# Optimization experiments

Hardware: AMD Instinct MI355X
Metric: run time of the kernel (lower is better)

Reference implementation:

```python
import jax, jax.numpy as jnp
import numpy as np

BLOCK_SIZE = 50  # from module globals


def setup_inputs() -> dict:
    key = jax.random.key(0)
    ks = jax.random.split(key, 5)
    B, T, C, H = 8, 1024, 512, 64
    return {
        "x": jax.random.normal(ks[0], (B, T, C), dtype=jnp.float32),
        "Wq": jax.random.normal(ks[1], (C, H), dtype=jnp.float32) * (C ** -0.5),
        "Wk": jax.random.normal(ks[2], (C, H), dtype=jnp.float32) * (C ** -0.5),
        "Wv": jax.random.normal(ks[3], (C, H), dtype=jnp.float32) * (C ** -0.5),
        "rel_pos_emb": jax.random.normal(ks[4], (2 * BLOCK_SIZE - 1, H), dtype=jnp.float32),
    }


def reference(x, Wq, Wk, Wv, rel_pos_emb):
    # x: [B, T, C]; dropout is identity in eval mode.
    B, T, C = x.shape
    q = x @ Wq  # [B, T, H]
    k = x @ Wk
    v = x @ Wv
    H = q.shape[-1]

    # relative position indices, clamped to window, shifted to [0, 2*block-2]
    t = jnp.arange(T)
    rel = jnp.clip(t[None, :] - t[:, None], -(BLOCK_SIZE - 1), BLOCK_SIZE - 1) + (BLOCK_SIZE - 1)
    E = rel_pos_emb[rel]  # [T, T, H]

    scale = H ** -0.5
    # content scores (scaled) + relative-position bias (unscaled, per source)
    wei = jnp.einsum("btd,bsd->bts", q, k) * scale + jnp.einsum("btd,tsd->bts", q, E)

    causal = t[None, :] <= t[:, None]  # [T, T] lower-triangular True
    wei = jnp.where(causal[None, :, :], wei, -jnp.inf)
    wei = jax.nn.softmax(wei, axis=-1)
    return jnp.einsum("bts,bsd->btd", wei, v)
```

## Files before the change

kernel.cpp:

```cpp
#include <hip/hip_runtime.h>
#include <hip/hip_bf16.h>

typedef __bf16 bf16x8 __attribute__((ext_vector_type(8)));
typedef float  f32x4  __attribute__((ext_vector_type(4)));

#define MFMA16(a, b, c) __builtin_amdgcn_mfma_f32_16x16x32_bf16(a, b, c, 0, 0, 0)

static __device__ __forceinline__ unsigned short bf16_bits(__bf16 v) {
    union { __bf16 b; unsigned short u; } x; x.b = v; return x.u;
}
static __device__ __forceinline__ f32x4 zero4() {
    f32x4 z = {0.f, 0.f, 0.f, 0.f}; return z;
}

__global__ void g_build_kernel(const float* __restrict__ Wq,
                               const float* __restrict__ rpe,
                               float* __restrict__ G) {
    int gid = blockIdx.x * 256 + threadIdx.x;
    int c = gid >> 6, j = gid & 63;
    const f32x4* wp = (const f32x4*)(Wq + c * 64);
    const f32x4* rp = (const f32x4*)(rpe + j * 64);
    float acc = 0.f;
#pragma unroll
    for (int i = 0; i < 16; i++) {
        f32x4 a = wp[i], b = rp[i];
        acc += a.x * b.x + a.y * b.y + a.z * b.z + a.w * b.w;
    }
    G[c * 64 + j] = acc;
}

__global__ void wt_build_kernel(const float* __restrict__ Wq,
                                const float* __restrict__ Wk,
                                const float* __restrict__ Wv,
                                const float* __restrict__ G,
                                __bf16* __restrict__ WT_hi,
                                __bf16* __restrict__ WT_lo) {
    int n = blockIdx.x;
    const float* src; int nc;
    if (n < 64)       { src = Wq; nc = n; }
    else if (n < 128) { src = Wk; nc = n - 64; }
    else if (n < 192) { src = Wv; nc = n - 128; }
    else              { src = G;  nc = n - 192; }
    int k = threadIdx.x * 2;
    float v0 = src[k * 64 + nc];
    float v1 = src[(k + 1) * 64 + nc];
    __bf16 h0 = (__bf16)v0, h1 = (__bf16)v1;
    WT_hi[n * 512 + k]     = h0;
    WT_hi[n * 512 + k + 1] = h1;
    WT_lo[n * 512 + k]     = (__bf16)(v0 - (float)h0);
    WT_lo[n * 512 + k + 1] = (__bf16)(v1 - (float)h1);
}

__global__ __launch_bounds__(256) void proj_kernel(
        const float* __restrict__ x,
        const __bf16* __restrict__ WT_hi, const __bf16* __restrict__ WT_lo,
        __bf16* __restrict__ qb, __bf16* __restrict__ kb,
        __bf16* __restrict__ vb, float* __restrict__ qE) {
    int tid = threadIdx.x;
    int lane = tid & 63, w = tid >> 6;
    int rt = w >> 1, ns = w & 1;
    int l15 = lane & 15, kg = lane >> 4;
    int rowA = blockIdx.x * 32 + rt * 16 + l15;
    const float* xrow = x + (size_t)rowA * 512;

    f32x4 acc[8];
#pragma unroll
    for (int i = 0; i < 8; i++) acc[i] = zero4();

    for (int ks = 0; ks < 16; ks++) {
        int k0 = ks * 32 + kg * 8;
        f32x4 a0 = *(const f32x4*)(xrow + k0);
        f32x4 a1 = *(const f32x4*)(xrow + k0 + 4);
        bf16x8 xh, xl;
#pragma unroll
        for (int e = 0; e < 4; e++) {
            float v = a0[e]; __bf16 h = (__bf16)v;
            xh[e] = h; xl[e] = (__bf16)(v - (float)h);
            v = a1[e]; h = (__bf16)v;
            xh[4 + e] = h; xl[4 + e] = (__bf16)(v - (float)h);
        }
#pragma unroll
        for (int i = 0; i < 8; i++) {
            int nt = ns + 2 * i;
            const __bf16* bp = WT_hi + (size_t)(nt * 16 + l15) * 512 + k0;
            bf16x8 bh = *(const bf16x8*)bp;
            acc[i] = MFMA16(xh, bh, acc[i]);
            if (nt < 4 || nt >= 12) {
                bf16x8 bl = *(const bf16x8*)(WT_lo + (size_t)(nt * 16 + l15) * 512 + k0);
                acc[i] = MFMA16(xh, bl, acc[i]);
                acc[i] = MFMA16(xl, bh, acc[i]);
            }
        }
    }
    int rowO = blockIdx.x * 32 + rt * 16 + kg * 4;
#pragma unroll
    for (int i = 0; i < 8; i++) {
        int nt = ns + 2 * i;
        int col = nt * 16 + l15;
#pragma unroll
        for (int r = 0; r < 4; r++) {
            float v = acc[i][r];
            int row = rowO + r;
            if (nt < 4) {
                qb[row * 64 + col] = (__bf16)v;
            } else if (nt < 12) {
                int c2 = col - 64;
                if (c2 < 64) kb[row * 64 + c2] = (__bf16)v;
                else         vb[row * 64 + (c2 - 64)] = (__bf16)v;
            } else {
                qE[row * 64 + (col - 192)] = v;
            }
        }
    }
}

__global__ __launch_bounds__(128) void attn_kernel(
        const __bf16* __restrict__ qb, const __bf16* __restrict__ kb,
        const __bf16* __restrict__ vb, const float* __restrict__ qE,
        float* __restrict__ out) {
    __shared__ __bf16 Klds[64][72];
    __shared__ __bf16 Vt[64][72];
    __shared__ __bf16 Plds[2][16][72];
    __shared__ float  qEs[32][50];

    int tid = threadIdx.x;
    int b = blockIdx.x & 7, tq = blockIdx.x >> 3;
    int bT = b * 1024;
    int lane = tid & 63, w = tid >> 6;
    int l15 = lane & 15, kg = lane >> 4;

    for (int idx = tid; idx < 32 * 50; idx += 128) {
        int r = idx / 50, j = idx - r * 50;
        qEs[r][j] = qE[(bT + tq * 32 + r) * 64 + j];
    }

    int qrow = bT + tq * 32 + w * 16 + l15;
    bf16x8 qf0 = *(const bf16x8*)(qb + (size_t)qrow * 64 + kg * 8);
    bf16x8 qf1 = *(const bf16x8*)(qb + (size_t)qrow * 64 + 32 + kg * 8);

    f32x4 O[4]; float m[4], ll[4];
#pragma unroll
    for (int i = 0; i < 4; i++) { O[i] = zero4(); m[i] = -1e30f; ll[i] = 0.f; }

    int ntiles = (tq >> 1) + 1;
    for (int it = 0; it < ntiles; it++) {
        int sb = it * 64;
        __syncthreads();
        {
            int row = tid >> 1, half = tid & 1;
            const __bf16* kp = kb + (size_t)(bT + sb + row) * 64 + half * 32;
#pragma unroll
            for (int i = 0; i < 4; i++)
                *(bf16x8*)&Klds[row][half * 32 + i * 8] = *(const bf16x8*)(kp + i * 8);
        }
        {
            int sp = (tid & 31) * 2, dseg = (tid >> 5) * 16;
            const __bf16* vp0 = vb + (size_t)(bT + sb + sp) * 64 + dseg;
            const __bf16* vp1 = vp0 + 64;
            bf16x8 r0a = *(const bf16x8*)vp0, r0b = *(const bf16x8*)(vp0 + 8);
            bf16x8 r1a = *(const bf16x8*)vp1, r1b = *(const bf16x8*)(vp1 + 8);
#pragma unroll
            for (int i = 0; i < 8; i++) {
                unsigned int p0 = (unsigned int)bf16_bits(r0a[i]) |
                                  ((unsigned int)bf16_bits(r1a[i]) << 16);
                *(unsigned int*)&Vt[dseg + i][sp] = p0;
                unsigned int p1 = (unsigned int)bf16_bits(r0b[i]) |
                                  ((unsigned int)bf16_bits(r1b[i]) << 16);
                *(unsigned int*)&Vt[dseg + 8 + i][sp] = p1;
            }
        }
        __syncthreads();

        f32x4 s[4];
#pragma unroll
        for (int ct = 0; ct < 4; ct++) {
            bf16x8 kf0 = *(const bf16x8*)&Klds[ct * 16 + l15][kg * 8];
            bf16x8 kf1 = *(const bf16x8*)&Klds[ct * 16 + l15][32 + kg * 8];
            f32x4 z = zero4();
            z = MFMA16(qf0, kf0, z);
            s[ct] = MFMA16(qf1, kf1, z);
        }

        float p[4][4];
        int trow0 = w * 16 + kg * 4;
#pragma unroll
        for (int r = 0; r < 4; r++) {
            int trow = trow0 + r;
            int tg = tq * 32 + trow;
            float mx = -1e30f;
#pragma unroll
            for (int ct = 0; ct < 4; ct++) {
                int sg = sb + ct * 16 + l15;
                int d = sg - tg;
                int idxj = (d < -49 ? -49 : d);
                idxj = (idxj > 0 ? 0 : idxj) + 49;
                float lg = s[ct][r] * 0.125f + qEs[trow][idxj];
                if (d > 0) lg = -1e30f;
                p[r][ct] = lg;
                mx = fmaxf(mx, lg);
            }
            mx = fmaxf(mx, __shfl_xor(mx, 1));
            mx = fmaxf(mx, __shfl_xor(mx, 2));
            mx = fmaxf(mx, __shfl_xor(mx, 4));
            mx = fmaxf(mx, __shfl_xor(mx, 8));
            float mnew = fmaxf(m[r], mx);
            float alpha = __expf(m[r] - mnew);
            m[r] = mnew;
            float ps = 0.f;
#pragma unroll
            for (int ct = 0; ct < 4; ct++) {
                float pv = __expf(p[r][ct] - mnew);
                p[r][ct] = pv;
                ps += pv;
            }
            ps += __shfl_xor(ps, 1);
            ps += __shfl_xor(ps, 2);
            ps += __shfl_xor(ps, 4);
            ps += __shfl_xor(ps, 8);
            ll[r] = ll[r] * alpha + ps;
#pragma unroll
            for (int dt = 0; dt < 4; dt++) O[dt][r] *= alpha;
        }

#pragma unroll
        for (int r = 0; r < 4; r++) {
            int prow = kg * 4 + r;
#pragma unroll
            for (int ct = 0; ct < 4; ct++)
                Plds[w][prow][ct * 16 + l15] = (__bf16)p[r][ct];
        }
        __syncthreads();

#pragma unroll
        for (int ks = 0; ks < 2; ks++) {
            bf16x8 af = *(const bf16x8*)&Plds[w][l15][ks * 32 + kg * 8];
#pragma unroll
            for (int dt = 0; dt < 4; dt++) {
                bf16x8 vf = *(const bf16x8*)&Vt[dt * 16 + l15][ks * 32 + kg * 8];
                O[dt] = MFMA16(af, vf, O[dt]);
            }
        }
    }

    int rowg = bT + tq * 32 + w * 16 + kg * 4;
#pragma unroll
    for (int dt = 0; dt < 4; dt++) {
#pragma unroll
        for (int r = 0; r < 4; r++) {
            out[(size_t)(rowg + r) * 64 + dt * 16 + l15] = O[dt][r] / ll[r];
        }
    }
}

extern "C" void kernel_launch(void* const* d_in, const int* in_sizes, int n_in,
                              void* d_out, int out_size, void* d_ws, size_t ws_size,
                              hipStream_t stream) {
    const float* x   = (const float*)d_in[0];
    const float* Wq  = (const float*)d_in[1];
    const float* Wk  = (const float*)d_in[2];
    const float* Wv  = (const float*)d_in[3];
    const float* rpe = (const float*)d_in[4];

    char* ws = (char*)d_ws;
    float*  G     = (float*)(ws);
    __bf16* WT_hi = (__bf16*)(ws + (128 << 10));
    __bf16* WT_lo = (__bf16*)(ws + (384 << 10));
    __bf16* qbuf  = (__bf16*)(ws + (640 << 10));
    __bf16* kbuf  = (__bf16*)(ws + (1664 << 10));
    __bf16* vbuf  = (__bf16*)(ws + (2688 << 10));
    float*  qE    = (float*)(ws + (3712 << 10));
    float*  outp  = (float*)d_out;

    hipLaunchKernelGGL(g_build_kernel,  dim3(128), dim3(256), 0, stream, Wq, rpe, G);
    hipLaunchKernelGGL(wt_build_kernel, dim3(256), dim3(256), 0, stream,
                       Wq, Wk, Wv, G, WT_hi, WT_lo);
    hipLaunchKernelGGL(proj_kernel,     dim3(256), dim3(256), 0, stream,
                       x, WT_hi, WT_lo, qbuf, kbuf, vbuf, qE);
    hipLaunchKernelGGL(attn_kernel,     dim3(256), dim3(128), 0, stream,
                       qbuf, kbuf, vbuf, qE, outp);
}
```

Measured before the change: 145.1 us.

## Fuse G build into weight prep, split projection finer, split-KV attention in-block

The Wq·rpe product is now computed inside the weight-transpose kernel, which removes one launch. The projection kernel uses 16-row blocks with each wave owning one output group, doubling the grid to 512 blocks. The attention kernel goes to 256 threads, with two wave pairs processing alternating KV tiles into double LDS buffers, and merges their partial softmax states through shared memory at the end. The aim is more parallelism in the causal attention loop, at the cost of extra LDS, the final merge step, and idle waves on odd tile counts.

New measurement: 126.5 us. 1.15x faster.

```diff
diff --git a/kernel.cpp b/kernel.cpp
--- a/kernel.cpp
+++ b/kernel.cpp
@@ -11,39 +11,38 @@
 }
 static __device__ __forceinline__ f32x4 zero4() {
     f32x4 z = {0.f, 0.f, 0.f, 0.f}; return z;
-}
-
-__global__ void g_build_kernel(const float* __restrict__ Wq,
-                               const float* __restrict__ rpe,
-                               float* __restrict__ G) {
-    int gid = blockIdx.x * 256 + threadIdx.x;
-    int c = gid >> 6, j = gid & 63;
-    const f32x4* wp = (const f32x4*)(Wq + c * 64);
-    const f32x4* rp = (const f32x4*)(rpe + j * 64);
-    float acc = 0.f;
-#pragma unroll
-    for (int i = 0; i < 16; i++) {
-        f32x4 a = wp[i], b = rp[i];
-        acc += a.x * b.x + a.y * b.y + a.z * b.z + a.w * b.w;
-    }
-    G[c * 64 + j] = acc;
 }
 
 __global__ void wt_build_kernel(const float* __restrict__ Wq,
                                 const float* __restrict__ Wk,
                                 const float* __restrict__ Wv,
-                                const float* __restrict__ G,
+                                const float* __restrict__ rpe,
                                 __bf16* __restrict__ WT_hi,
                                 __bf16* __restrict__ WT_lo) {
     int n = blockIdx.x;
-    const float* src; int nc;
-    if (n < 64)       { src = Wq; nc = n; }
-    else if (n < 128) { src = Wk; nc = n - 64; }
-    else if (n < 192) { src = Wv; nc = n - 128; }
-    else              { src = G;  nc = n - 192; }
     int k = threadIdx.x * 2;
-    float v0 = src[k * 64 + nc];
-    float v1 = src[(k + 1) * 64 + nc];
+    float v0, v1;
+    if (n < 192) {
+        const float* src; int nc;
+        if (n < 64)       { src = Wq; nc = n; }
+        else if (n < 128) { src = Wk; nc = n - 64; }
+        else              { src = Wv; nc = n - 128; }
+        v0 = src[k * 64 + nc];
+        v1 = src[(k + 1) * 64 + nc];
+    } else {
+        int nc = n - 192;
+        const f32x4* rp = (const f32x4*)(rpe + nc * 64);
+        const f32x4* w0 = (const f32x4*)(Wq + k * 64);
+        const f32x4* w1 = (const f32x4*)(Wq + (k + 1) * 64);
+        float a0 = 0.f, a1 = 0.f;
+#pragma unroll
+        for (int i = 0; i < 16; i++) {
+            f32x4 r = rp[i], x0 = w0[i], x1 = w1[i];
+            a0 += x0.x * r.x + x0.y * r.y + x0.z * r.z + x0.w * r.w;
+            a1 += x1.x * r.x + x1.y * r.y + x1.z * r.z + x1.w * r.w;
+        }
+        v0 = a0; v1 = a1;
+    }
     __bf16 h0 = (__bf16)v0, h1 = (__bf16)v1;
     WT_hi[n * 512 + k]     = h0;
     WT_hi[n * 512 + k + 1] = h1;
@@ -57,16 +56,16 @@
         __bf16* __restrict__ qb, __bf16* __restrict__ kb,
         __bf16* __restrict__ vb, float* __restrict__ qE) {
     int tid = threadIdx.x;
-    int lane = tid & 63, w = tid >> 6;
-    int rt = w >> 1, ns = w & 1;
+    int lane = tid & 63, c = tid >> 6;
     int l15 = lane & 15, kg = lane >> 4;
-    int rowA = blockIdx.x * 32 + rt * 16 + l15;
+    int rowA = blockIdx.x * 16 + l15;
     const float* xrow = x + (size_t)rowA * 512;
 
-    f32x4 acc[8];
-#pragma unroll
-    for (int i = 0; i < 8; i++) acc[i] = zero4();
-
+    f32x4 acc[4];
+#pragma unroll
+    for (int i = 0; i < 4; i++) acc[i] = zero4();
+
+#pragma unroll
     for (int ks = 0; ks < 16; ks++) {
         int k0 = ks * 32 + kg * 8;
         f32x4 a0 = *(const f32x4*)(xrow + k0);
@@ -80,61 +79,60 @@
             xh[4 + e] = h; xl[4 + e] = (__bf16)(v - (float)h);
         }
 #pragma unroll
-        for (int i = 0; i < 8; i++) {
-            int nt = ns + 2 * i;
+        for (int i = 0; i < 4; i++) {
+            int nt = c + 4 * i;
             const __bf16* bp = WT_hi + (size_t)(nt * 16 + l15) * 512 + k0;
             bf16x8 bh = *(const bf16x8*)bp;
             acc[i] = MFMA16(xh, bh, acc[i]);
-            if (nt < 4 || nt >= 12) {
+            if (i == 0 || i == 3) {
                 bf16x8 bl = *(const bf16x8*)(WT_lo + (size_t)(nt * 16 + l15) * 512 + k0);
                 acc[i] = MFMA16(xh, bl, acc[i]);
                 acc[i] = MFMA16(xl, bh, acc[i]);
             }
         }
     }
-    int rowO = blockIdx.x * 32 + rt * 16 + kg * 4;
-#pragma unroll
-    for (int i = 0; i < 8; i++) {
-        int nt = ns + 2 * i;
-        int col = nt * 16 + l15;
+    int rowO = blockIdx.x * 16 + kg * 4;
+#pragma unroll
+    for (int i = 0; i < 4; i++) {
+        int col = (c + 4 * i) * 16 + l15;
+        int cc = col & 63;
 #pragma unroll
         for (int r = 0; r < 4; r++) {
             float v = acc[i][r];
             int row = rowO + r;
-            if (nt < 4) {
-                qb[row * 64 + col] = (__bf16)v;
-            } else if (nt < 12) {
-                int c2 = col - 64;
-                if (c2 < 64) kb[row * 64 + c2] = (__bf16)v;
-                else         vb[row * 64 + (c2 - 64)] = (__bf16)v;
-            } else {
-                qE[row * 64 + (col - 192)] = v;
-            }
-        }
-    }
-}
-
-__global__ __launch_bounds__(128) void attn_kernel(
+            if (i == 0)      qb[row * 64 + cc] = (__bf16)v;
+            else if (i == 1) kb[row * 64 + cc] = (__bf16)v;
+            else if (i == 2) vb[row * 64 + cc] = (__bf16)v;
+            else             qE[row * 64 + cc] = v;
+        }
+    }
+}
+
+__global__ __launch_bounds__(256) void attn_kernel(
         const __bf16* __restrict__ qb, const __bf16* __restrict__ kb,
         const __bf16* __restrict__ vb, const float* __restrict__ qE,
         float* __restrict__ out) {
-    __shared__ __bf16 Klds[64][72];
-    __shared__ __bf16 Vt[64][72];
-    __shared__ __bf16 Plds[2][16][72];
+    __shared__ __bf16 Klds[2][64][72];
+    __shared__ __bf16 Vt[2][64][72];
+    __shared__ __bf16 Plds[4][16][72];
     __shared__ float  qEs[32][50];
+    __shared__ float  Oc[2][16][66];
+    __shared__ float  mc[2][16], lc[2][16];
 
     int tid = threadIdx.x;
     int b = blockIdx.x & 7, tq = blockIdx.x >> 3;
     int bT = b * 1024;
     int lane = tid & 63, w = tid >> 6;
+    int rh = w >> 1, kvq = w & 1;
     int l15 = lane & 15, kg = lane >> 4;
-
-    for (int idx = tid; idx < 32 * 50; idx += 128) {
+    int ptid = rh * 64 + lane;
+
+    for (int idx = tid; idx < 32 * 50; idx += 256) {
         int r = idx / 50, j = idx - r * 50;
         qEs[r][j] = qE[(bT + tq * 32 + r) * 64 + j];
     }
 
-    int qrow = bT + tq * 32 + w * 16 + l15;
+    int qrow = bT + tq * 32 + rh * 16 + l15;
     bf16x8 qf0 = *(const bf16x8*)(qb + (size_t)qrow * 64 + kg * 8);
     bf16x8 qf1 = *(const bf16x8*)(qb + (size_t)qrow * 64 + 32 + kg * 8);
 
@@ -143,46 +141,53 @@
     for (int i = 0; i < 4; i++) { O[i] = zero4(); m[i] = -1e30f; ll[i] = 0.f; }
 
     int ntiles = (tq >> 1) + 1;
-    for (int it = 0; it < ntiles; it++) {
+    int R = (ntiles + 1) >> 1;
+    for (int rr = 0; rr < R; rr++) {
+        int it = rr * 2 + kvq;
+        int active = (it < ntiles);
         int sb = it * 64;
         __syncthreads();
-        {
-            int row = tid >> 1, half = tid & 1;
-            const __bf16* kp = kb + (size_t)(bT + sb + row) * 64 + half * 32;
-#pragma unroll
-            for (int i = 0; i < 4; i++)
-                *(bf16x8*)&Klds[row][half * 32 + i * 8] = *(const bf16x8*)(kp + i * 8);
-        }
-        {
-            int sp = (tid & 31) * 2, dseg = (tid >> 5) * 16;
-            const __bf16* vp0 = vb + (size_t)(bT + sb + sp) * 64 + dseg;
-            const __bf16* vp1 = vp0 + 64;
-            bf16x8 r0a = *(const bf16x8*)vp0, r0b = *(const bf16x8*)(vp0 + 8);
-            bf16x8 r1a = *(const bf16x8*)vp1, r1b = *(const bf16x8*)(vp1 + 8);
-#pragma unroll
-            for (int i = 0; i < 8; i++) {
-                unsigned int p0 = (unsigned int)bf16_bits(r0a[i]) |
-                                  ((unsigned int)bf16_bits(r1a[i]) << 16);
-                *(unsigned int*)&Vt[dseg + i][sp] = p0;
-                unsigned int p1 = (unsigned int)bf16_bits(r0b[i]) |
-                                  ((unsigned int)bf16_bits(r1b[i]) << 16);
-                *(unsigned int*)&Vt[dseg + 8 + i][sp] = p1;
+        if (active) {
+            {
+                int row = ptid >> 1, half = ptid & 1;
+                const __bf16* kp = kb + (size_t)(bT + sb + row) * 64 + half * 32;
+#pragma unroll
+                for (int i = 0; i < 4; i++)
+                    *(bf16x8*)&Klds[kvq][row][half * 32 + i * 8] =
+                        *(const bf16x8*)(kp + i * 8);
+            }
+            {
+                int sp = (ptid & 31) * 2, dseg = (ptid >> 5) * 16;
+                const __bf16* vp0 = vb + (size_t)(bT + sb + sp) * 64 + dseg;
+                const __bf16* vp1 = vp0 + 64;
+                bf16x8 r0a = *(const bf16x8*)vp0, r0b = *(const bf16x8*)(vp0 + 8);
+                bf16x8 r1a = *(const bf16x8*)vp1, r1b = *(const bf16x8*)(vp1 + 8);
+#pragma unroll
+                for (int i = 0; i < 8; i++) {
+                    unsigned int p0 = (unsigned int)bf16_bits(r0a[i]) |
+                                      ((unsigned int)bf16_bits(r1a[i]) << 16);
+                    *(unsigned int*)&Vt[kvq][dseg + i][sp] = p0;
+                    unsigned int p1 = (unsigned int)bf16_bits(r0b[i]) |
+                                      ((unsigned int)bf16_bits(r1b[i]) << 16);
+                    *(unsigned int*)&Vt[kvq][dseg + 8 + i][sp] = p1;
+                }
             }
         }
         __syncthreads();
+        if (!active) continue;
 
         f32x4 s[4];
 #pragma unroll
         for (int ct = 0; ct < 4; ct++) {
-            bf16x8 kf0 = *(const bf16x8*)&Klds[ct * 16 + l15][kg * 8];
-            bf16x8 kf1 = *(const bf16x8*)&Klds[ct * 16 + l15][32 + kg * 8];
+            bf16x8 kf0 = *(const bf16x8*)&Klds[kvq][ct * 16 + l15][kg * 8];
+            bf16x8 kf1 = *(const bf16x8*)&Klds[kvq][ct * 16 + l15][32 + kg * 8];
             f32x4 z = zero4();
             z = MFMA16(qf0, kf0, z);
             s[ct] = MFMA16(qf1, kf1, z);
         }
 
         float p[4][4];
-        int trow0 = w * 16 + kg * 4;
+        int trow0 = rh * 16 + kg * 4;
 #pragma unroll
         for (int r = 0; r < 4; r++) {
             int trow = trow0 + r;
@@ -229,25 +234,51 @@
             for (int ct = 0; ct < 4; ct++)
                 Plds[w][prow][ct * 16 + l15] = (__bf16)p[r][ct];
         }
-        __syncthreads();
 
 #pragma unroll
         for (int ks = 0; ks < 2; ks++) {
             bf16x8 af = *(const bf16x8*)&Plds[w][l15][ks * 32 + kg * 8];
 #pragma unroll
             for (int dt = 0; dt < 4; dt++) {
-                bf16x8 vf = *(const bf16x8*)&Vt[dt * 16 + l15][ks * 32 + kg * 8];
+                bf16x8 vf = *(const bf16x8*)&Vt[kvq][dt * 16 + l15][ks * 32 + kg * 8];
                 O[dt] = MFMA16(af, vf, O[dt]);
             }
         }
     }
 
-    int rowg = bT + tq * 32 + w * 16 + kg * 4;
-#pragma unroll
-    for (int dt = 0; dt < 4; dt++) {
-#pragma unroll
-        for (int r = 0; r < 4; r++) {
-            out[(size_t)(rowg + r) * 64 + dt * 16 + l15] = O[dt][r] / ll[r];
+    __syncthreads();
+    if (kvq == 1) {
+#pragma unroll
+        for (int r = 0; r < 4; r++) {
+            int row = kg * 4 + r;
+            if (l15 == 0) { mc[rh][row] = m[r]; lc[rh][row] = ll[r]; }
+#pragma unroll
+            for (int dt = 0; dt < 4; dt++)
+                Oc[rh][row][dt * 16 + l15] = O[dt][r];
+        }
+    }
+    __syncthreads();
+    if (kvq == 0) {
+        int rowg = bT + tq * 32 + rh * 16 + kg * 4;
+#pragma unroll
+        for (int r = 0; r < 4; r++) {
+            int row = kg * 4 + r;
+            float mB = mc[rh][row], lB = lc[rh][row];
+            float ms = fmaxf(m[r], mB);
+            float a = __expf(m[r] - ms), bb = __expf(mB - ms);
+            float denom = a * ll[r] + bb * lB;
+            float inv = 1.0f / denom;
+#pragma unroll
+            for (int dt = 0; dt < 4; dt++) {
+#pragma unroll
+                for (int e = 0; e < 4; e++) {
+                }
+            }
+#pragma unroll
+            for (int dt = 0; dt < 4; dt++) {
+                float val = (a * O[dt][r] + bb * Oc[rh][row][dt * 16 + l15]) * inv;
+                out[(size_t)(rowg + r) * 64 + dt * 16 + l15] = val;
+            }
         }
     }
 }
@@ -262,20 +293,18 @@
     const float* rpe = (const float*)d_in[4];
 
     char* ws = (char*)d_ws;
-    float*  G     = (float*)(ws);
-    __bf16* WT_hi = (__bf16*)(ws + (128 << 10));
-    __bf16* WT_lo = (__bf16*)(ws + (384 << 10));
-    __bf16* qbuf  = (__bf16*)(ws + (640 << 10));
-    __bf16* kbuf  = (__bf16*)(ws + (1664 << 10));
-    __bf16* vbuf  = (__bf16*)(ws + (2688 << 10));
-    float*  qE    = (float*)(ws + (3712 << 10));
+    __bf16* WT_hi = (__bf16*)(ws);
+    __bf16* WT_lo = (__bf16*)(ws + (256 << 10));
+    __bf16* qbuf  = (__bf16*)(ws + (512 << 10));
+    __bf16* kbuf  = (__bf16*)(ws + (1536 << 10));
+    __bf16* vbuf  = (__bf16*)(ws + (2560 << 10));
+    float*  qE    = (float*)(ws + (3584 << 10));
     float*  outp  = (float*)d_out;
 
-    hipLaunchKernelGGL(g_build_kernel,  dim3(128), dim3(256), 0, stream, Wq, rpe, G);
     hipLaunchKernelGGL(wt_build_kernel, dim3(256), dim3(256), 0, stream,
-                       Wq, Wk, Wv, G, WT_hi, WT_lo);
-    hipLaunchKernelGGL(proj_kernel,     dim3(256), dim3(256), 0, stream,
+                       Wq, Wk, Wv, rpe, WT_hi, WT_lo);
+    hipLaunchKernelGGL(proj_kernel,     dim3(512), dim3(256), 0, stream,
                        x, WT_hi, WT_lo, qbuf, kbuf, vbuf, qE);
-    hipLaunchKernelGGL(attn_kernel,     dim3(256), dim3(128), 0, stream,
+    hipLaunchKernelGGL(attn_kernel,     dim3(256), dim3(256), 0, stream,
                        qbuf, kbuf, vbuf, qE, outp);
 }
```
